# Kernel optimization log

Hardware: AMD Instinct MI355X
Metric: run time of the kernel (lower is better)

The kernel has to match this reference:

```python
import jax, jax.numpy as jnp
import numpy as np

TEMPERATURE = 0.07
B, D = 8192, 1024
EPS = 1e-08


def setup_inputs() -> dict:
    key = jax.random.key(0)
    k1, k2, k3, k4, k5 = jax.random.split(key, 5)
    visual_feats = jax.random.normal(k1, (B, D), dtype=jnp.float32)
    textual_feats = jax.random.normal(k2, (B, D), dtype=jnp.float32)
    transport_matrix = jax.random.uniform(k3, (B, B), dtype=jnp.float32)
    confident_clean_mask = jax.random.randint(k4, (B,), 0, 2).astype(jnp.bool_)
    confident_noisy_mask = jax.random.randint(k5, (B,), 0, 2).astype(jnp.bool_)
    return {
        'visual_feats': visual_feats,
        'textual_feats': textual_feats,
        'transport_matrix': transport_matrix,
        'confident_clean_mask': confident_clean_mask,
        'confident_noisy_mask': confident_noisy_mask,
    }


def _l2norm(x):
    # matches F.normalize(p=2, dim=-1) with default eps=1e-12
    n = jnp.sqrt(jnp.sum(x * x, axis=-1, keepdims=True))
    return x / jnp.maximum(n, 1e-12)


def reference(visual_feats, textual_feats, transport_matrix,
              confident_clean_mask, confident_noisy_mask):
    # current_epoch defaults to 0 < push_phase_epochs -> 'push_only' phase:
    # progressive_loss = CCL complementary (negative-push) loss.
    n = confident_noisy_mask.astype(jnp.float32)  # [B]
    # negative_mask[i,j] = 1 if (i==j and noisy[i]) or (i!=j and (noisy[i] or noisy[j]))
    # at i==j, max(n[i],n[i]) == n[i], so the broadcast max covers both cases.
    negative_mask = jnp.maximum(n[:, None], n[None, :])  # [B, B]

    v = _l2norm(visual_feats)
    t = _l2norm(textual_feats)
    similarities = v @ t.T  # [B, B]

    logits = similarities / TEMPERATURE
    neg_sum = jnp.sum(jnp.exp(logits) * negative_mask, axis=1) + EPS  # [B]
    progressive_loss = jnp.mean(jnp.log(neg_sum))
    return progressive_loss
```

## Files before the change

kernel.cpp:

```cpp
#include <hip/hip_runtime.h>
#include <hip/hip_bf16.h>

#define NB 8192
#define ND 1024

typedef __attribute__((ext_vector_type(8))) short bf16x8;
typedef __attribute__((ext_vector_type(4))) float f32x4;

__device__ __forceinline__ void async16(const void* g, void* l) {
  __builtin_amdgcn_global_load_lds(
      (const __attribute__((address_space(1))) void*)g,
      (__attribute__((address_space(3))) void*)l,
      16, 0, 0);
}

__device__ __forceinline__ unsigned ldsaddr(const void* p) {
  return (unsigned)(size_t)(const __attribute__((address_space(3))) void*)p;
}

template <int IMM>
__device__ __forceinline__ bf16x8 dsr(unsigned a) {
  bf16x8 r;
  asm volatile("ds_read_b128 %0, %1 offset:%2" : "=v"(r) : "v"(a), "i"(IMM));
  return r;
}

__device__ __forceinline__ unsigned short f2bf(float f) {
  union { float f; unsigned u; } a; a.f = f;
  unsigned u = a.u;
  return (unsigned short)((u + 0x7fffu + ((u >> 16) & 1u)) >> 16);
}

__global__ void prep_mask(const unsigned char* __restrict__ raw,
                          float* __restrict__ nmask) {
  __shared__ int flag;
  if (threadIdx.x == 0) flag = 0;
  __syncthreads();
  int any = 0;
  for (int i = threadIdx.x; i < NB; i += 256)
    if ((i & 3) != 0 && raw[i] != 0) any = 1;
  if (any) atomicOr(&flag, 1);
  __syncthreads();
  if (flag) {
    for (int i = threadIdx.x; i < NB; i += 256)
      nmask[i] = raw[i] ? 1.0f : 0.0f;
  } else {
    const int* ri = (const int*)raw;
    for (int i = threadIdx.x; i < NB; i += 256)
      nmask[i] = ri[i] ? 1.0f : 0.0f;
  }
}

__global__ void norm_cast(const float* __restrict__ vis,
                          const float* __restrict__ txt,
                          unsigned short* __restrict__ vb,
                          unsigned short* __restrict__ tb) {
  const float* src = blockIdx.y ? txt : vis;
  unsigned short* dst = blockIdx.y ? tb : vb;
  int row = blockIdx.x;
  int t = threadIdx.x;
  float4 x = ((const float4*)(src + (size_t)row * ND))[t];
  float ss = x.x * x.x + x.y * x.y + x.z * x.z + x.w * x.w;
  #pragma unroll
  for (int m = 32; m; m >>= 1) ss += __shfl_xor(ss, m);
  __shared__ float sred[4];
  if ((t & 63) == 0) sred[t >> 6] = ss;
  __syncthreads();
  float tot = sred[0] + sred[1] + sred[2] + sred[3];
  float inv = 1.0f / fmaxf(sqrtf(tot), 1e-12f);
  ushort4 o;
  o.x = f2bf(x.x * inv); o.y = f2bf(x.y * inv);
  o.z = f2bf(x.z * inv); o.w = f2bf(x.w * inv);
  ((ushort4*)dst)[(size_t)row * (ND / 4) + t] = o;
}

#define AS_BARRIER asm volatile("s_barrier" ::: "memory")
#define LGKM0 do { asm volatile("s_waitcnt lgkmcnt(0)" ::: "memory"); \
                   __builtin_amdgcn_sched_barrier(0); } while (0)
#define VMCNT(n) asm volatile("s_waitcnt vmcnt(" #n ")" ::: "memory")

#define STG(GB, LB, KT, H) do {                                               \
    async16(GB + (size_t)((H) * 128 + 0) * ND + (KT) * 64,                    \
            LB + ((H) * 128 + 0) * 128);                                      \
    async16(GB + (size_t)((H) * 128 + 64) * ND + (KT) * 64,                   \
            LB + ((H) * 128 + 64) * 128);                                     \
  } while (0)

#define RDA(BUF, MH, DST) do {                                                \
    DST[0][0] = dsr<(BUF)*32768 + (MH)*8192 + 0   >(aA0);                     \
    DST[0][1] = dsr<(BUF)*32768 + (MH)*8192 + 0   >(aA1);                     \
    DST[1][0] = dsr<(BUF)*32768 + (MH)*8192 + 2048>(aA0);                     \
    DST[1][1] = dsr<(BUF)*32768 + (MH)*8192 + 2048>(aA1);                     \
    DST[2][0] = dsr<(BUF)*32768 + (MH)*8192 + 4096>(aA0);                     \
    DST[2][1] = dsr<(BUF)*32768 + (MH)*8192 + 4096>(aA1);                     \
    DST[3][0] = dsr<(BUF)*32768 + (MH)*8192 + 6144>(aA0);                     \
    DST[3][1] = dsr<(BUF)*32768 + (MH)*8192 + 6144>(aA1);                     \
  } while (0)

#define RDB(BUF) do {                                                         \
    b[0][0] = dsr<(BUF)*32768 + 0   >(aB0);                                   \
    b[0][1] = dsr<(BUF)*32768 + 0   >(aB1);                                   \
    b[1][0] = dsr<(BUF)*32768 + 2048>(aB0);                                   \
    b[1][1] = dsr<(BUF)*32768 + 2048>(aB1);                                   \
    b[2][0] = dsr<(BUF)*32768 + 4096>(aB0);                                   \
    b[2][1] = dsr<(BUF)*32768 + 4096>(aB1);                                   \
    b[3][0] = dsr<(BUF)*32768 + 6144>(aB0);                                   \
    b[3][1] = dsr<(BUF)*32768 + 6144>(aB1);                                   \
  } while (0)

#define MFMAQ(AF, RB, NH) do {                                                \
    _Pragma("unroll") for (int mi_ = 0; mi_ < 4; ++mi_)                       \
    _Pragma("unroll") for (int ni_ = 0; ni_ < 2; ++ni_)                       \
    _Pragma("unroll") for (int kk_ = 0; kk_ < 2; ++kk_)                       \
      acc[(RB) + mi_][(NH)*2 + ni_] =                                         \
          __builtin_amdgcn_mfma_f32_16x16x32_bf16(                            \
              AF[mi_][kk_], b[(NH)*2 + ni_][kk_],                             \
              acc[(RB) + mi_][(NH)*2 + ni_], 0, 0, 0);                        \
  } while (0)

__global__ __launch_bounds__(512, 2) void gemm_fused(
    const unsigned short* __restrict__ vb, const unsigned short* __restrict__ tb,
    const float* __restrict__ nmask, float* __restrict__ partial) {
  __shared__ unsigned short As[2][256 * 64];
  __shared__ unsigned short Bs[2][256 * 64];
  __shared__ float part[256][4];

  int lin = blockIdx.y * 32 + blockIdx.x;
  lin = (lin & 7) * 128 + (lin >> 3);
  const int bx = lin & 31, by = lin >> 5;
  const int i0 = by * 256, j0 = bx * 256;

  const int t = threadIdx.x;
  const int w = t >> 6, l = t & 63;
  const int quad = l >> 4, l15 = l & 15;
  const int wm = w >> 2, wn = w & 3;

  const int lrow = l >> 3;
  const int lch = (l & 7) ^ lrow;
  const unsigned short* Ag = vb + (size_t)(i0 + w * 8 + lrow) * ND + lch * 8;
  const unsigned short* Bg = tb + (size_t)(j0 + w * 8 + lrow) * ND + lch * 8;
  char* AL0 = (char*)&As[0][0] + w * 1024;
  char* AL1 = (char*)&As[1][0] + w * 1024;
  char* BL0 = (char*)&Bs[0][0] + w * 1024;
  char* BL1 = (char*)&Bs[1][0] + w * 1024;

  const int rA = wm * 128 + l15;
  const int rB = wn * 64 + l15;
  const int c0 = quad ^ (l & 7);
  const unsigned aA0 = ldsaddr(&As[0][0]) + rA * 128 + c0 * 16;
  const unsigned aA1 = aA0 ^ 64;
  const unsigned aB0 = ldsaddr(&Bs[0][0]) + rB * 128 + c0 * 16;
  const unsigned aB1 = aB0 ^ 64;

  STG(Ag, AL0, 0, 0); STG(Ag, AL0, 0, 1);
  STG(Bg, BL0, 0, 0); STG(Bg, BL0, 0, 1);
  STG(Ag, AL1, 1, 0); STG(Ag, AL1, 1, 1);
  VMCNT(4);
  AS_BARRIER;

  bf16x8 a[4][2], a2[4][2], b[4][2];
  f32x4 acc[8][4] = {};

  #pragma unroll 1
  for (int tt = 0; tt < 8; ++tt) {
    const int k0 = 2 * tt, k1 = 2 * tt + 1;
    const bool pf = (tt < 7);
    RDB(0); RDA(0, 0, a);
    STG(Bg, BL1, k1, 0);
    AS_BARRIER; LGKM0;
    __builtin_amdgcn_s_setprio(1); MFMAQ(a, 0, 0); __builtin_amdgcn_s_setprio(0);
    AS_BARRIER;
    RDA(0, 1, a2);
    STG(Bg, BL1, k1, 1);
    AS_BARRIER; LGKM0;
    __builtin_amdgcn_s_setprio(1); MFMAQ(a, 0, 1); __builtin_amdgcn_s_setprio(0);
    AS_BARRIER;
    if (pf) STG(Ag, AL0, k0 + 2, 0);
    AS_BARRIER;
    __builtin_amdgcn_s_setprio(1); MFMAQ(a2, 4, 0); __builtin_amdgcn_s_setprio(0);
    AS_BARRIER;
    if (pf) { STG(Ag, AL0, k0 + 2, 1); VMCNT(4); } else { VMCNT(0); }
    AS_BARRIER;
    __builtin_amdgcn_s_setprio(1); MFMAQ(a2, 4, 1); __builtin_amdgcn_s_setprio(0);
    AS_BARRIER;
    RDB(1); RDA(1, 0, a);
    if (pf) STG(Bg, BL0, k0 + 2, 0);
    AS_BARRIER; LGKM0;
    __builtin_amdgcn_s_setprio(1); MFMAQ(a, 0, 0); __builtin_amdgcn_s_setprio(0);
    AS_BARRIER;
    RDA(1, 1, a2);
    if (pf) STG(Bg, BL0, k0 + 2, 1);
    AS_BARRIER; LGKM0;
    __builtin_amdgcn_s_setprio(1); MFMAQ(a, 0, 1); __builtin_amdgcn_s_setprio(0);
    AS_BARRIER;
    if (pf) STG(Ag, AL1, k1 + 2, 0);
    AS_BARRIER;
    __builtin_amdgcn_s_setprio(1); MFMAQ(a2, 4, 0); __builtin_amdgcn_s_setprio(0);
    AS_BARRIER;
    if (pf) { STG(Ag, AL1, k1 + 2, 1); VMCNT(4); }
    AS_BARRIER;
    __builtin_amdgcn_s_setprio(1); MFMAQ(a2, 4, 1); __builtin_amdgcn_s_setprio(0);
    AS_BARRIER;
  }

  const float SCALE = 20.60992915555662f;
  float ncol[4];
  #pragma unroll
  for (int ni = 0; ni < 4; ++ni) ncol[ni] = nmask[j0 + wn * 64 + ni * 16 + l15];

  #pragma unroll
  for (int mi = 0; mi < 8; ++mi) {
    float nrow[4], ra[4] = {0.f, 0.f, 0.f, 0.f};
    #pragma unroll
    for (int r = 0; r < 4; ++r)
      nrow[r] = nmask[i0 + wm * 128 + mi * 16 + quad * 4 + r];
    #pragma unroll
    for (int ni = 0; ni < 4; ++ni)
      #pragma unroll
      for (int r = 0; r < 4; ++r)
        ra[r] += exp2f(acc[mi][ni][r] * SCALE) * fmaxf(nrow[r], ncol[ni]);
    #pragma unroll
    for (int r = 0; r < 4; ++r) {
      float v = ra[r];
      v += __shfl_xor(v, 1); v += __shfl_xor(v, 2);
      v += __shfl_xor(v, 4); v += __shfl_xor(v, 8);
      if (l15 == 0) part[wm * 128 + mi * 16 + quad * 4 + r][wn] = v;
    }
  }
  __syncthreads();
  if (t < 256)
    partial[(size_t)bx * NB + i0 + t] =
        part[t][0] + part[t][1] + part[t][2] + part[t][3];
}

__global__ void finalize(const float* __restrict__ partial, float* __restrict__ out) {
  int r = blockIdx.x * 256 + threadIdx.x;
  float s = 0.f;
  #pragma unroll 4
  for (int c = 0; c < 32; ++c) s += partial[(size_t)c * NB + r];
  float lg = logf(s + 1e-8f);
  #pragma unroll
  for (int m = 32; m; m >>= 1) lg += __shfl_xor(lg, m);
  __shared__ float sred[4];
  if ((threadIdx.x & 63) == 0) sred[threadIdx.x >> 6] = lg;
  __syncthreads();
  if (threadIdx.x == 0)
    atomicAdd(out, (sred[0] + sred[1] + sred[2] + sred[3]) * (1.0f / NB));
}

extern "C" void kernel_launch(void* const* d_in, const int* in_sizes, int n_in,
                              void* d_out, int out_size, void* d_ws, size_t ws_size,
                              hipStream_t stream) {
  const float* vis = (const float*)d_in[0];
  const float* txt = (const float*)d_in[1];
  const unsigned char* noisy = (const unsigned char*)d_in[4];
  float* out = (float*)d_out;

  char* ws = (char*)d_ws;
  unsigned short* vb = (unsigned short*)ws;
  unsigned short* tb = (unsigned short*)(ws + ((size_t)16 << 20));
  float* nmask = (float*)(ws + ((size_t)32 << 20));
  float* partial = (float*)(ws + ((size_t)32 << 20) + (64 << 10));

  hipMemsetAsync(d_out, 0, sizeof(float), stream);
  prep_mask<<<1, 256, 0, stream>>>(noisy, nmask);
  norm_cast<<<dim3(NB, 2), 256, 0, stream>>>(vis, txt, vb, tb);
  gemm_fused<<<dim3(NB / 256, NB / 256), 512, 0, stream>>>(vb, tb, nmask, partial);
  finalize<<<NB / 256, 256, 0, stream>>>(partial, out);
}
```

Baseline: 497.3 us.

## Software-pipeline LDS fragment reads under MFMA phases in GEMM main loop

Moves the LDS reads of A and B fragments so they are issued before the preceding MFMA batch, with scheduling fences, instead of right after a barrier. Part of the B fragments is read after the last MFMA batch of each half-iteration, and the first tile's fragments are loaded before the loop. The aim is to hide LDS read latency behind matrix-core work rather than stalling on lgkmcnt. The risks are data hazards if reads run ahead of the barriers that publish the async-staged buffers, and more register pressure from fragments held live.

```diff
diff --git a/kernel.cpp b/kernel.cpp
--- a/kernel.cpp
+++ b/kernel.cpp
@@ -78,6 +78,7 @@
 #define LGKM0 do { asm volatile("s_waitcnt lgkmcnt(0)" ::: "memory"); \
                    __builtin_amdgcn_sched_barrier(0); } while (0)
 #define VMCNT(n) asm volatile("s_waitcnt vmcnt(" #n ")" ::: "memory")
+#define SCHED_FENCE __builtin_amdgcn_sched_barrier(0)
 
 #define STG(GB, LB, KT, H) do {                                               \
     async16(GB + (size_t)((H) * 128 + 0) * ND + (KT) * 64,                    \
@@ -97,11 +98,14 @@
     DST[3][1] = dsr<(BUF)*32768 + (MH)*8192 + 6144>(aA1);                     \
   } while (0)
 
-#define RDB(BUF) do {                                                         \
+#define RDB01(BUF) do {                                                       \
     b[0][0] = dsr<(BUF)*32768 + 0   >(aB0);                                   \
     b[0][1] = dsr<(BUF)*32768 + 0   >(aB1);                                   \
     b[1][0] = dsr<(BUF)*32768 + 2048>(aB0);                                   \
     b[1][1] = dsr<(BUF)*32768 + 2048>(aB1);                                   \
+  } while (0)
+
+#define RDB23(BUF) do {                                                       \
     b[2][0] = dsr<(BUF)*32768 + 4096>(aB0);                                   \
     b[2][1] = dsr<(BUF)*32768 + 4096>(aB1);                                   \
     b[3][0] = dsr<(BUF)*32768 + 6144>(aB0);                                   \
@@ -118,6 +122,9 @@
               acc[(RB) + mi_][(NH)*2 + ni_], 0, 0, 0);                        \
   } while (0)
 
+#define PRIO1 __builtin_amdgcn_s_setprio(1)
+#define PRIO0 __builtin_amdgcn_s_setprio(0)
+
 __global__ __launch_bounds__(512, 2) void gemm_fused(
     const unsigned short* __restrict__ vb, const unsigned short* __restrict__ tb,
     const float* __restrict__ nmask, float* __restrict__ partial) {
@@ -161,45 +168,56 @@
   bf16x8 a[4][2], a2[4][2], b[4][2];
   f32x4 acc[8][4] = {};
 
+  RDA(0, 0, a); RDB01(0); RDB23(0);
+  SCHED_FENCE;
+
   #pragma unroll 1
   for (int tt = 0; tt < 8; ++tt) {
     const int k0 = 2 * tt, k1 = 2 * tt + 1;
     const bool pf = (tt < 7);
-    RDB(0); RDA(0, 0, a);
     STG(Bg, BL1, k1, 0);
     AS_BARRIER; LGKM0;
-    __builtin_amdgcn_s_setprio(1); MFMAQ(a, 0, 0); __builtin_amdgcn_s_setprio(0);
-    AS_BARRIER;
     RDA(0, 1, a2);
+    SCHED_FENCE;
+    PRIO1; MFMAQ(a, 0, 0); PRIO0;
+    AS_BARRIER;
     STG(Bg, BL1, k1, 1);
     AS_BARRIER; LGKM0;
-    __builtin_amdgcn_s_setprio(1); MFMAQ(a, 0, 1); __builtin_amdgcn_s_setprio(0);
+    PRIO1; MFMAQ(a, 0, 1); PRIO0;
     AS_BARRIER;
     if (pf) STG(Ag, AL0, k0 + 2, 0);
     AS_BARRIER;
-    __builtin_amdgcn_s_setprio(1); MFMAQ(a2, 4, 0); __builtin_amdgcn_s_setprio(0);
+    PRIO1; MFMAQ(a2, 4, 0); PRIO0;
     AS_BARRIER;
     if (pf) { STG(Ag, AL0, k0 + 2, 1); VMCNT(4); } else { VMCNT(0); }
     AS_BARRIER;
-    __builtin_amdgcn_s_setprio(1); MFMAQ(a2, 4, 1); __builtin_amdgcn_s_setprio(0);
-    AS_BARRIER;
-    RDB(1); RDA(1, 0, a);
+    RDA(1, 0, a); RDB01(1);
+    SCHED_FENCE;
+    PRIO1; MFMAQ(a2, 4, 1); PRIO0;
+    SCHED_FENCE;
+    RDB23(1);
+    AS_BARRIER;
     if (pf) STG(Bg, BL0, k0 + 2, 0);
     AS_BARRIER; LGKM0;
-    __builtin_amdgcn_s_setprio(1); MFMAQ(a, 0, 0); __builtin_amdgcn_s_setprio(0);
-    AS_BARRIER;
     RDA(1, 1, a2);
+    SCHED_FENCE;
+    PRIO1; MFMAQ(a, 0, 0); PRIO0;
+    AS_BARRIER;
     if (pf) STG(Bg, BL0, k0 + 2, 1);
     AS_BARRIER; LGKM0;
-    __builtin_amdgcn_s_setprio(1); MFMAQ(a, 0, 1); __builtin_amdgcn_s_setprio(0);
+    PRIO1; MFMAQ(a, 0, 1); PRIO0;
     AS_BARRIER;
     if (pf) STG(Ag, AL1, k1 + 2, 0);
     AS_BARRIER;
-    __builtin_amdgcn_s_setprio(1); MFMAQ(a2, 4, 0); __builtin_amdgcn_s_setprio(0);
+    PRIO1; MFMAQ(a2, 4, 0); PRIO0;
     AS_BARRIER;
     if (pf) { STG(Ag, AL1, k1 + 2, 1); VMCNT(4); }
     AS_BARRIER;
-    __builtin_amdgcn_s_setprio(1); MFMAQ(a2, 4, 1); __builtin_amdgcn_s_setprio(0);
+    if (pf) { RDA(0, 0, a); RDB01(0); }
+    SCHED_FENCE;
+    PRIO1; MFMAQ(a2, 4, 1); PRIO0;
+    SCHED_FENCE;
+    if (pf) RDB23(0);
     AS_BARRIER;
   }
 
```

After: 486.0 us. 2.3% less time.
